# Kernel optimization log

Measured on AMD Instinct MI355X. Metric: run time of the kernel, lower is better.

Reference implementation:

```python
import jax, jax.numpy as jnp
import numpy as np

GAMMA = 2          # relu(cos_sim)**gamma, from init gamma=2
EPS = 1e-8         # torch CosineSimilarity eps (norm clamp)
B, C, H, WID = 4, 256, 64, 64


def setup_inputs() -> dict:
    key = jax.random.key(0)
    kx, kw = jax.random.split(key)
    x = jax.random.normal(kx, (B, C, H, WID), dtype=jnp.float32)
    # 1x1 conv (nlayers=1): weight [C_out, C_in], bias [C_out]
    W = jax.random.normal(kw, (C, C), dtype=jnp.float32) * 0.02
    b = jnp.zeros((C,), dtype=jnp.float32)
    return {"x": x, "W": W, "b": b}


def reference(x, W, b):
    # x: [B,C,H,W]. Flatten pixels: p/q index (h*W+w).
    Bs, Cs, Hs, Ws = x.shape
    xf = x.reshape(Bs, Cs, Hs * Ws)                      # [B,C,P]
    norm = jnp.sqrt(jnp.sum(xf * xf, axis=1, keepdims=True))
    xn = xf / jnp.maximum(norm, EPS)                     # channel-normalized
    # full pairwise cosine similarity over pixels, relu, power gamma
    s = jax.nn.relu(jnp.einsum('bcp,bcq->bpq', xn, xn)) ** GAMMA  # [B,P,Q]
    # transform: 1x1 conv = per-pixel linear map over channels
    gx = jnp.einsum('oc,bcp->bop', W, xf) + b[None, :, None]      # [B,C,P]
    # y[b,c,p] = sum_q s[b,p,q] * gx[b,c,q]  (== 'bijhw,bchw->bcij')
    y = jnp.einsum('bpq,bcq->bcp', s, gx)
    return y.reshape(Bs, Cs, Hs, Ws)
```

## Files before the change

### kernel.cpp

```cpp
#include <hip/hip_runtime.h>

#define BN 4
#define CN 256
#define PN 4096
#define QT 64
#define TSTR 264

typedef __attribute__((ext_vector_type(8))) short short8;
typedef __attribute__((ext_vector_type(8))) unsigned short ushort8;
typedef __attribute__((ext_vector_type(4))) float f32x4;
typedef __attribute__((ext_vector_type(4))) unsigned int u32x4;
typedef unsigned int u32;

__device__ __forceinline__ unsigned short f2bf(float f) {
  u32 u = __builtin_bit_cast(u32, f);
  return (unsigned short)((u + 0x7fffu + ((u >> 16) & 1u)) >> 16);
}

__device__ __forceinline__ void async_copy16(const void* g, void* l) {
  __builtin_amdgcn_global_load_lds((const __attribute__((address_space(1))) u32*)g,
                                   (__attribute__((address_space(3))) u32*)l, 16, 0, 0);
}


__global__ __launch_bounds__(256) void k_nx(const float* __restrict__ x,
                                            float* __restrict__ mnorm,
                                            unsigned short* __restrict__ xnK) {
  __shared__ unsigned short tl[64 * TSTR];
  __shared__ float red[4][64];
  const int b = blockIdx.y, qb = blockIdx.x, p0 = qb * 64;
  const int tid = threadIdx.x;
  const int tp = tid & 63, cg = tid >> 6;
  const float* xp = x + ((size_t)b * CN + cg * 64) * PN + p0 + tp;
  float v[64];
  float ss = 0.f;
#pragma unroll
  for (int i = 0; i < 64; ++i) {
    v[i] = xp[(size_t)i * PN];
    ss += v[i] * v[i];
  }
  red[cg][tp] = ss;
  __syncthreads();
  float nrm = sqrtf(red[0][tp] + red[1][tp] + red[2][tp] + red[3][tp]);
  float mn = fmaxf(nrm, 1e-8f);
  float rn = 1.f / mn;
  if (cg == 0) mnorm[b * PN + p0 + tp] = mn;
  unsigned int* tl32 = (unsigned int*)tl;
#pragma unroll
  for (int j = 0; j < 32; ++j) {
    unsigned int w = (unsigned int)f2bf(v[2 * j] * rn) |
                     ((unsigned int)f2bf(v[2 * j + 1] * rn) << 16);
    tl32[tp * (TSTR / 2) + cg * 32 + j] = w;
  }
  __syncthreads();
  char* dstb = (char*)xnK + (size_t)b * (PN * CN * 2) + (size_t)qb * 32768;
#pragma unroll
  for (int m = 0; m < 8; ++m) {
    int idx = m * 256 + tid;
    int F = idx >> 6, ln = idx & 63;
    int pl = (F >> 3) * 16 + (ln & 15);
    int ch = (F & 7) * 32 + (ln >> 4) * 8;
    ushort8 o = *(const ushort8*)(tl + pl * TSTR + ch);
    *(ushort8*)(dstb + (size_t)idx * 16) = o;
  }
}

__global__ void k_gx(const float* __restrict__ Wm, const float* __restrict__ bias,
                     const unsigned short* __restrict__ xnK, const float* __restrict__ mnorm,
                     unsigned short* __restrict__ gxF) {
  const int b = blockIdx.z;
  const int m0 = blockIdx.y * 64;
  const int qb = blockIdx.x, q0 = qb * 64;
  const int tid = threadIdx.x;
  const int wave = tid >> 6, lane = tid & 63;
  const int lr = lane & 15, g = lane >> 4;

  short8 af[8];
  {
    const float* wr = Wm + (size_t)(m0 + wave * 16 + lr) * CN;
#pragma unroll
    for (int k = 0; k < 8; ++k) {
      const float* ap = wr + k * 32 + g * 8;
      short8 a;
#pragma unroll
      for (int j = 0; j < 8; ++j) a[j] = (short)f2bf(ap[j]);
      af[k] = a;
    }
  }
  f32x4 acc[4];
#pragma unroll
  for (int n = 0; n < 4; ++n) acc[n] = (f32x4){0.f, 0.f, 0.f, 0.f};

  const char* xb = (const char*)xnK + (size_t)b * (PN * CN * 2) + (size_t)qb * 32768;
#pragma unroll
  for (int n = 0; n < 4; ++n)
#pragma unroll
    for (int k = 0; k < 8; ++k) {
      short8 bf = *(const short8*)(xb + ((n * 8 + k) << 10) + ((g * 16 + lr) << 4));
      acc[n] = __builtin_amdgcn_mfma_f32_16x16x32_bf16(af[k], bf, acc[n], 0, 0, 0);
    }
  char* vbb = (char*)gxF + (size_t)b * (PN * CN * 2) + (size_t)qb * 32768;
#pragma unroll
  for (int n = 0; n < 4; ++n) {
    int q = q0 + n * 16 + lr;
    float mn = mnorm[b * PN + q];
    int kk = n >> 1;
    int q32 = (n & 1) * 16 + lr;
    int gp = (q32 >> 2) & 3;
    int j = ((q32 >> 4) & 1) * 4 + (q32 & 3);
#pragma unroll
    for (int i = 0; i < 4; ++i) {
      int c = m0 + wave * 16 + g * 4 + i;
      float v = acc[n][i] * mn + bias[c];
      *(unsigned short*)(vbb + ((kk * 16 + (c >> 4)) << 10) + (gp << 8) + ((c & 15) << 4) + (j << 1)) = f2bf(v);
    }
  }
}

extern __shared__ char smem[];

__global__ __launch_bounds__(512, 2) void k_attn(const unsigned short* __restrict__ xnK,
                                                 const unsigned short* __restrict__ gxF,
                                                 float* __restrict__ d0, float* __restrict__ d1,
                                                 float* __restrict__ d2, float* __restrict__ d3,
                                                 int lq, int ntiles) {
  const int fid = blockIdx.x;
  const int b = fid & 3;
  const int qs = (fid >> 2) & ((1 << lq) - 1);
  const int pblk = fid >> (2 + lq);
  const int tid = threadIdx.x;
  const int wave = tid >> 6, lane = tid & 63, lr = lane & 15, g = lane >> 4;
  const int qb0 = (qs * (PN >> lq)) >> 6;
  const int p0 = pblk * 256 + wave * 32;
  float* dst = (qs == 0) ? d0 : (qs == 1) ? d1 : (qs == 2) ? d2 : d3;

  const char* xb = (const char*)xnK + (size_t)b * (PN * CN * 2);
  const char* vg = (const char*)gxF + (size_t)b * (PN * CN * 2);
  const char* kq = xb + (size_t)qb0 * 32768;
  const char* vq = vg + (size_t)qb0 * 32768;
  const int ldst = tid * 16;
  const int lane16 = lane * 16;

  auto issue_K = [&](int t) {
    char* kb = smem + (t & 1) * 65536;
    const char* s = kq + (size_t)t * 32768 + ldst;
#pragma unroll
    for (int j = 0; j < 4; ++j) async_copy16(s + j * 8192, kb + ldst + j * 8192);
  };
  auto issue_V = [&](int t) {
    char* vb = smem + (t & 1) * 65536 + 32768;
    const char* s = vq + (size_t)t * 32768 + ldst;
#pragma unroll
    for (int j = 0; j < 4; ++j) async_copy16(s + j * 8192, vb + ldst + j * 8192);
  };

  issue_K(0);
  issue_V(0);

  short8 qf[2][8];
  {
    const char* qpb = xb + (size_t)(pblk * 4 + (wave >> 1)) * 32768;
#pragma unroll
    for (int mt = 0; mt < 2; ++mt) {
      int ntp = (wave & 1) * 2 + mt;
#pragma unroll
      for (int k = 0; k < 8; ++k)
        qf[mt][k] = *(const short8*)(qpb + ((ntp * 8 + k) << 10) + ((g * 16 + lr) << 4));
    }
  }

  f32x4 yacc[2][16];
#pragma unroll
  for (int mt = 0; mt < 2; ++mt)
#pragma unroll
    for (int n = 0; n < 16; ++n) yacc[mt][n] = (f32x4){0.f, 0.f, 0.f, 0.f};

  for (int t = 0; t < ntiles; ++t) {
    const char* kb = smem + (t & 1) * 65536;
    const char* vb = kb + 32768;

    asm volatile("s_waitcnt vmcnt(4)" ::: "memory");
    __builtin_amdgcn_s_barrier();
    if (t + 1 < ntiles) { issue_K(t + 1); issue_V(t + 1); }

    u32 pa[2][2][4];
#pragma unroll
    for (int nh = 0; nh < 2; ++nh) {
      f32x4 sacc[2][2];
#pragma unroll
      for (int n0 = 0; n0 < 2; ++n0)
#pragma unroll
        for (int mt = 0; mt < 2; ++mt) sacc[n0][mt] = (f32x4){0.f, 0.f, 0.f, 0.f};
      __builtin_amdgcn_s_setprio(1);
#pragma unroll
      for (int k = 0; k < 8; ++k) {
        short8 kf0 = *(const short8*)(kb + ((2 * nh) * 8 + k) * 1024 + lane16);
        short8 kf1 = *(const short8*)(kb + ((2 * nh + 1) * 8 + k) * 1024 + lane16);
        sacc[0][0] = __builtin_amdgcn_mfma_f32_16x16x32_bf16(kf0, qf[0][k], sacc[0][0], 0, 0, 0);
        sacc[0][1] = __builtin_amdgcn_mfma_f32_16x16x32_bf16(kf0, qf[1][k], sacc[0][1], 0, 0, 0);
        sacc[1][0] = __builtin_amdgcn_mfma_f32_16x16x32_bf16(kf1, qf[0][k], sacc[1][0], 0, 0, 0);
        sacc[1][1] = __builtin_amdgcn_mfma_f32_16x16x32_bf16(kf1, qf[1][k], sacc[1][1], 0, 0, 0);
      }
      __builtin_amdgcn_s_setprio(0);
#pragma unroll
      for (int mt = 0; mt < 2; ++mt)
#pragma unroll
        for (int n0 = 0; n0 < 2; ++n0)
#pragma unroll
          for (int h = 0; h < 2; ++h) {
            float a0 = fmaxf(sacc[n0][mt][2 * h], 0.f);
            a0 *= a0;
            float a1 = fmaxf(sacc[n0][mt][2 * h + 1], 0.f);
            a1 *= a1;
            u32 w;
            asm("v_cvt_pk_bf16_f32 %0, %1, %2" : "=v"(w) : "v"(a0), "v"(a1));
            pa[mt][nh][n0 * 2 + h] = w;
          }
    }

    if (t + 1 < ntiles) {
      asm volatile("s_waitcnt vmcnt(8)" ::: "memory");
    } else {
      asm volatile("s_waitcnt vmcnt(0)" ::: "memory");
    }
    __builtin_amdgcn_s_barrier();

#pragma unroll
    for (int kk = 0; kk < 2; ++kk) {
      u32x4 w0 = {pa[0][kk][0], pa[0][kk][1], pa[0][kk][2], pa[0][kk][3]};
      u32x4 w1 = {pa[1][kk][0], pa[1][kk][1], pa[1][kk][2], pa[1][kk][3]};
      short8 a0 = __builtin_bit_cast(short8, w0);
      short8 a1 = __builtin_bit_cast(short8, w1);
      __builtin_amdgcn_s_setprio(1);
#pragma unroll
      for (int n2 = 0; n2 < 16; ++n2) {
        short8 vf = *(const short8*)(vb + (kk * 16 + n2) * 1024 + lane16);
        yacc[0][n2] = __builtin_amdgcn_mfma_f32_16x16x32_bf16(a0, vf, yacc[0][n2], 0, 0, 0);
        yacc[1][n2] = __builtin_amdgcn_mfma_f32_16x16x32_bf16(a1, vf, yacc[1][n2], 0, 0, 0);
      }
      __builtin_amdgcn_s_setprio(0);
    }
  }
  __builtin_amdgcn_s_barrier();

  float* yl = (float*)(smem + wave * 16384);
  const int row8 = lane >> 3, p4 = (lane & 7) << 2;
#pragma unroll
  for (int cc = 0; cc < 4; ++cc) {
#pragma unroll
    for (int nn = 0; nn < 4; ++nn)
#pragma unroll
      for (int mt = 0; mt < 2; ++mt)
#pragma unroll
        for (int i = 0; i < 4; ++i)
          yl[(nn * 16 + lr) * 33 + mt * 16 + g * 4 + i] = yacc[mt][cc * 4 + nn][i];
#pragma unroll
    for (int r2 = 0; r2 < 8; ++r2) {
      int c = r2 * 8 + row8;
      float4 v = *(const float4*)(yl + c * 33 + p4);
      *(float4*)(dst + ((size_t)b * CN + cc * 64 + c) * PN + p0 + p4) = v;
    }
  }
}

__global__ void k_add(float* __restrict__ o, const float* __restrict__ a,
                      const float* __restrict__ bb, const float* __restrict__ c,
                      int np, int n4) {
  int i = blockIdx.x * blockDim.x + threadIdx.x;
  int stride = gridDim.x * blockDim.x;
  float4* o4 = (float4*)o;
  const float4* a4 = (const float4*)a;
  const float4* b4 = (const float4*)bb;
  const float4* c4 = (const float4*)c;
  for (; i < n4; i += stride) {
    float4 r = o4[i];
    float4 va = a4[i];
    r.x += va.x; r.y += va.y; r.z += va.z; r.w += va.w;
    if (np > 1) {
      float4 vb = b4[i];
      r.x += vb.x; r.y += vb.y; r.z += vb.z; r.w += vb.w;
      float4 vc = c4[i];
      r.x += vc.x; r.y += vc.y; r.z += vc.z; r.w += vc.w;
    }
    o4[i] = r;
  }
}

extern "C" void kernel_launch(void* const* d_in, const int* in_sizes, int n_in,
                              void* d_out, int out_size, void* d_ws, size_t ws_size,
                              hipStream_t stream) {
  const float* x = (const float*)d_in[0];
  const float* Wm = (const float*)d_in[1];
  const float* bias = (const float*)d_in[2];
  float* out = (float*)d_out;

  char* ws = (char*)d_ws;
  unsigned short* xnK = (unsigned short*)ws;
  unsigned short* gxF = (unsigned short*)(ws + (size_t)8388608);
  float* mnorm = (float*)(ws + (size_t)16777216);
  float* yp0 = (float*)(ws + (size_t)16842752);
  float* yp1 = yp0 + 4194304;
  float* yp2 = yp1 + 4194304;
  const size_t need4 = 16842752ULL + 3ULL * 16777216ULL;

  hipFuncSetAttribute(reinterpret_cast<const void*>(k_attn),
                      hipFuncAttributeMaxDynamicSharedMemorySize, 131072);

  k_nx<<<dim3(PN / 64, BN), 256, 0, stream>>>(x, mnorm, xnK);
  k_gx<<<dim3(PN / 64, CN / 64, BN), 256, 0, stream>>>(Wm, bias, xnK, mnorm, gxF);
  if (ws_size >= need4) {
    k_attn<<<dim3(256), 512, 131072, stream>>>(xnK, gxF, out, yp0, yp1, yp2, 2, (PN / 4) / QT);
    k_add<<<dim3(1024), 256, 0, stream>>>(out, yp0, yp1, yp2, 3, BN * CN * PN / 4);
  } else {
    k_attn<<<dim3(128), 512, 131072, stream>>>(xnK, gxF, out, yp0, yp0, yp0, 1, (PN / 2) / QT);
    k_add<<<dim3(1024), 256, 0, stream>>>(out, yp0, yp0, yp0, 1, BN * CN * PN / 4);
  }
}
```

Before: 101.1 us.

## Fuse normalize and 1x1 conv kernels; store split-Q partials in fp16

Merges the normalization kernel and the conv-transform kernel into one. Each block computes the gx tile from its bf16 normalized tile already in LDS, with norms kept in shared memory, instead of re-reading xnK and mnorm from global. The split-Q attention partials are now written as fp16 into four workspace buffers rather than fp32 into the output plus three buffers. The final add kernel converts and sums all four, which roughly halves the partial-sum traffic and removes a launch. The cost is fp16 precision and range on the partial outputs, and each block in the fused kernel now does the whole 256-channel GEMM, with fewer blocks than the old k_gx grid.

```diff
diff --git a/kernel.cpp b/kernel.cpp
--- a/kernel.cpp
+++ b/kernel.cpp
@@ -1,4 +1,5 @@
 #include <hip/hip_runtime.h>
+#include <hip/hip_fp16.h>
 
 #define BN 4
 #define CN 256
@@ -8,6 +9,7 @@
 
 typedef __attribute__((ext_vector_type(8))) short short8;
 typedef __attribute__((ext_vector_type(8))) unsigned short ushort8;
+typedef __attribute__((ext_vector_type(4))) unsigned short us4;
 typedef __attribute__((ext_vector_type(4))) float f32x4;
 typedef __attribute__((ext_vector_type(4))) unsigned int u32x4;
 typedef unsigned int u32;
@@ -23,96 +25,99 @@
 }
 
 
-__global__ __launch_bounds__(256) void k_nx(const float* __restrict__ x,
-                                            float* __restrict__ mnorm,
-                                            unsigned short* __restrict__ xnK) {
+__global__ __launch_bounds__(256) void k_nxgx(const float* __restrict__ x,
+                                              const float* __restrict__ Wm,
+                                              const float* __restrict__ bias,
+                                              unsigned short* __restrict__ xnK,
+                                              unsigned short* __restrict__ gxF) {
   __shared__ unsigned short tl[64 * TSTR];
   __shared__ float red[4][64];
+  __shared__ float mnl[64];
   const int b = blockIdx.y, qb = blockIdx.x, p0 = qb * 64;
   const int tid = threadIdx.x;
   const int tp = tid & 63, cg = tid >> 6;
-  const float* xp = x + ((size_t)b * CN + cg * 64) * PN + p0 + tp;
-  float v[64];
-  float ss = 0.f;
-#pragma unroll
-  for (int i = 0; i < 64; ++i) {
-    v[i] = xp[(size_t)i * PN];
-    ss += v[i] * v[i];
-  }
-  red[cg][tp] = ss;
-  __syncthreads();
-  float nrm = sqrtf(red[0][tp] + red[1][tp] + red[2][tp] + red[3][tp]);
-  float mn = fmaxf(nrm, 1e-8f);
-  float rn = 1.f / mn;
-  if (cg == 0) mnorm[b * PN + p0 + tp] = mn;
-  unsigned int* tl32 = (unsigned int*)tl;
-#pragma unroll
-  for (int j = 0; j < 32; ++j) {
-    unsigned int w = (unsigned int)f2bf(v[2 * j] * rn) |
-                     ((unsigned int)f2bf(v[2 * j + 1] * rn) << 16);
-    tl32[tp * (TSTR / 2) + cg * 32 + j] = w;
-  }
-  __syncthreads();
-  char* dstb = (char*)xnK + (size_t)b * (PN * CN * 2) + (size_t)qb * 32768;
-#pragma unroll
-  for (int m = 0; m < 8; ++m) {
-    int idx = m * 256 + tid;
-    int F = idx >> 6, ln = idx & 63;
-    int pl = (F >> 3) * 16 + (ln & 15);
-    int ch = (F & 7) * 32 + (ln >> 4) * 8;
-    ushort8 o = *(const ushort8*)(tl + pl * TSTR + ch);
-    *(ushort8*)(dstb + (size_t)idx * 16) = o;
-  }
-}
-
-__global__ void k_gx(const float* __restrict__ Wm, const float* __restrict__ bias,
-                     const unsigned short* __restrict__ xnK, const float* __restrict__ mnorm,
-                     unsigned short* __restrict__ gxF) {
-  const int b = blockIdx.z;
-  const int m0 = blockIdx.y * 64;
-  const int qb = blockIdx.x, q0 = qb * 64;
-  const int tid = threadIdx.x;
+
+  {
+    const float* xp = x + ((size_t)b * CN + cg * 64) * PN + p0 + tp;
+    float v[64];
+    float ss = 0.f;
+#pragma unroll
+    for (int i = 0; i < 64; ++i) {
+      v[i] = xp[(size_t)i * PN];
+      ss += v[i] * v[i];
+    }
+    red[cg][tp] = ss;
+    __syncthreads();
+    float nrm = sqrtf(red[0][tp] + red[1][tp] + red[2][tp] + red[3][tp]);
+    float mn = fmaxf(nrm, 1e-8f);
+    float rn = 1.f / mn;
+    if (cg == 0) mnl[tp] = mn;
+    unsigned int* tl32 = (unsigned int*)tl;
+#pragma unroll
+    for (int j = 0; j < 32; ++j) {
+      unsigned int w = (unsigned int)f2bf(v[2 * j] * rn) |
+                       ((unsigned int)f2bf(v[2 * j + 1] * rn) << 16);
+      tl32[tp * (TSTR / 2) + cg * 32 + j] = w;
+    }
+    __syncthreads();
+    char* dstb = (char*)xnK + (size_t)b * (PN * CN * 2) + (size_t)qb * 32768;
+#pragma unroll
+    for (int m = 0; m < 8; ++m) {
+      int idx = m * 256 + tid;
+      int F = idx >> 6, ln = idx & 63;
+      int pl = (F >> 3) * 16 + (ln & 15);
+      int ch = (F & 7) * 32 + (ln >> 4) * 8;
+      ushort8 o = *(const ushort8*)(tl + pl * TSTR + ch);
+      *(ushort8*)(dstb + (size_t)idx * 16) = o;
+    }
+  }
+
   const int wave = tid >> 6, lane = tid & 63;
   const int lr = lane & 15, g = lane >> 4;
-
-  short8 af[8];
-  {
-    const float* wr = Wm + (size_t)(m0 + wave * 16 + lr) * CN;
-#pragma unroll
-    for (int k = 0; k < 8; ++k) {
-      const float* ap = wr + k * 32 + g * 8;
-      short8 a;
-#pragma unroll
-      for (int j = 0; j < 8; ++j) a[j] = (short)f2bf(ap[j]);
-      af[k] = a;
-    }
-  }
-  f32x4 acc[4];
-#pragma unroll
-  for (int n = 0; n < 4; ++n) acc[n] = (f32x4){0.f, 0.f, 0.f, 0.f};
-
-  const char* xb = (const char*)xnK + (size_t)b * (PN * CN * 2) + (size_t)qb * 32768;
-#pragma unroll
-  for (int n = 0; n < 4; ++n)
-#pragma unroll
-    for (int k = 0; k < 8; ++k) {
-      short8 bf = *(const short8*)(xb + ((n * 8 + k) << 10) + ((g * 16 + lr) << 4));
-      acc[n] = __builtin_amdgcn_mfma_f32_16x16x32_bf16(af[k], bf, acc[n], 0, 0, 0);
-    }
   char* vbb = (char*)gxF + (size_t)b * (PN * CN * 2) + (size_t)qb * 32768;
 #pragma unroll
-  for (int n = 0; n < 4; ++n) {
-    int q = q0 + n * 16 + lr;
-    float mn = mnorm[b * PN + q];
-    int kk = n >> 1;
-    int q32 = (n & 1) * 16 + lr;
-    int gp = (q32 >> 2) & 3;
-    int j = ((q32 >> 4) & 1) * 4 + (q32 & 3);
-#pragma unroll
-    for (int i = 0; i < 4; ++i) {
-      int c = m0 + wave * 16 + g * 4 + i;
-      float v = acc[n][i] * mn + bias[c];
-      *(unsigned short*)(vbb + ((kk * 16 + (c >> 4)) << 10) + (gp << 8) + ((c & 15) << 4) + (j << 1)) = f2bf(v);
+  for (int mp = 0; mp < 2; ++mp) {
+    short8 af[2][8];
+#pragma unroll
+    for (int mt = 0; mt < 2; ++mt) {
+      const float* wr = Wm + (size_t)(wave * 64 + mp * 32 + mt * 16 + lr) * CN;
+#pragma unroll
+      for (int k = 0; k < 8; ++k) {
+        const float* ap = wr + k * 32 + g * 8;
+        short8 a;
+#pragma unroll
+        for (int j = 0; j < 8; ++j) a[j] = (short)f2bf(ap[j]);
+        af[mt][k] = a;
+      }
+    }
+    f32x4 acc[2][4];
+#pragma unroll
+    for (int mt = 0; mt < 2; ++mt)
+#pragma unroll
+      for (int n = 0; n < 4; ++n) acc[mt][n] = (f32x4){0.f, 0.f, 0.f, 0.f};
+#pragma unroll
+    for (int n = 0; n < 4; ++n)
+#pragma unroll
+      for (int k = 0; k < 8; ++k) {
+        short8 bf = *(const short8*)((const char*)tl + (n * 16 + lr) * (TSTR * 2) + k * 64 + g * 16);
+        acc[0][n] = __builtin_amdgcn_mfma_f32_16x16x32_bf16(af[0][k], bf, acc[0][n], 0, 0, 0);
+        acc[1][n] = __builtin_amdgcn_mfma_f32_16x16x32_bf16(af[1][k], bf, acc[1][n], 0, 0, 0);
+      }
+#pragma unroll
+    for (int n = 0; n < 4; ++n) {
+      float mn = mnl[n * 16 + lr];
+      int kk = n >> 1;
+      int q32 = (n & 1) * 16 + lr;
+      int gp = (q32 >> 2) & 3;
+      int j = ((q32 >> 4) & 1) * 4 + (q32 & 3);
+#pragma unroll
+      for (int mt = 0; mt < 2; ++mt)
+#pragma unroll
+        for (int i = 0; i < 4; ++i) {
+          int c = wave * 64 + mp * 32 + mt * 16 + g * 4 + i;
+          float v = acc[mt][n][i] * mn + bias[c];
+          *(unsigned short*)(vbb + ((kk * 16 + (c >> 4)) << 10) + (gp << 8) + ((c & 15) << 4) + (j << 1)) = f2bf(v);
+        }
     }
   }
 }
@@ -121,8 +126,8 @@
 
 __global__ __launch_bounds__(512, 2) void k_attn(const unsigned short* __restrict__ xnK,
                                                  const unsigned short* __restrict__ gxF,
-                                                 float* __restrict__ d0, float* __restrict__ d1,
-                                                 float* __restrict__ d2, float* __restrict__ d3,
+                                                 __half* __restrict__ p0h, __half* __restrict__ p1h,
+                                                 __half* __restrict__ p2h, __half* __restrict__ p3h,
                                                  int lq, int ntiles) {
   const int fid = blockIdx.x;
   const int b = fid & 3;
@@ -132,7 +137,7 @@
   const int wave = tid >> 6, lane = tid & 63, lr = lane & 15, g = lane >> 4;
   const int qb0 = (qs * (PN >> lq)) >> 6;
   const int p0 = pblk * 256 + wave * 32;
-  float* dst = (qs == 0) ? d0 : (qs == 1) ? d1 : (qs == 2) ? d2 : d3;
+  __half* dsth = (qs == 0) ? p0h : (qs == 1) ? p1h : (qs == 2) ? p2h : p3h;
 
   const char* xb = (const char*)xnK + (size_t)b * (PN * CN * 2);
   const char* vg = (const char*)gxF + (size_t)b * (PN * CN * 2);
@@ -208,10 +213,8 @@
         for (int n0 = 0; n0 < 2; ++n0)
 #pragma unroll
           for (int h = 0; h < 2; ++h) {
-            float a0 = fmaxf(sacc[n0][mt][2 * h], 0.f);
-            a0 *= a0;
-            float a1 = fmaxf(sacc[n0][mt][2 * h + 1], 0.f);
-            a1 *= a1;
+            float a0 = fmaxf(sacc[n0][mt][2 * h], 0.f); a0 *= a0;
+            float a1 = fmaxf(sacc[n0][mt][2 * h + 1], 0.f); a1 *= a1;
             u32 w;
             asm("v_cvt_pk_bf16_f32 %0, %1, %2" : "=v"(w) : "v"(a0), "v"(a1));
             pa[mt][nh][n0 * 2 + h] = w;
@@ -258,29 +261,41 @@
     for (int r2 = 0; r2 < 8; ++r2) {
       int c = r2 * 8 + row8;
       float4 v = *(const float4*)(yl + c * 33 + p4);
-      *(float4*)(dst + ((size_t)b * CN + cc * 64 + c) * PN + p0 + p4) = v;
-    }
-  }
-}
-
-__global__ void k_add(float* __restrict__ o, const float* __restrict__ a,
-                      const float* __restrict__ bb, const float* __restrict__ c,
-                      int np, int n4) {
+      size_t off = ((size_t)b * CN + cc * 64 + c) * PN + p0 + p4;
+      us4 h;
+      h[0] = __builtin_bit_cast(unsigned short, __float2half(v.x));
+      h[1] = __builtin_bit_cast(unsigned short, __float2half(v.y));
+      h[2] = __builtin_bit_cast(unsigned short, __float2half(v.z));
+      h[3] = __builtin_bit_cast(unsigned short, __float2half(v.w));
+      *(us4*)(dsth + off) = h;
+    }
+  }
+}
+
+__global__ void k_add(float* __restrict__ o, const uint2* __restrict__ a,
+                      const uint2* __restrict__ bb, const uint2* __restrict__ c,
+                      const uint2* __restrict__ d, int np, int n4) {
   int i = blockIdx.x * blockDim.x + threadIdx.x;
   int stride = gridDim.x * blockDim.x;
   float4* o4 = (float4*)o;
-  const float4* a4 = (const float4*)a;
-  const float4* b4 = (const float4*)bb;
-  const float4* c4 = (const float4*)c;
   for (; i < n4; i += stride) {
-    float4 r = o4[i];
-    float4 va = a4[i];
-    r.x += va.x; r.y += va.y; r.z += va.z; r.w += va.w;
-    if (np > 1) {
-      float4 vb = b4[i];
-      r.x += vb.x; r.y += vb.y; r.z += vb.z; r.w += vb.w;
-      float4 vc = c4[i];
-      r.x += vc.x; r.y += vc.y; r.z += vc.z; r.w += vc.w;
+    uint2 ua = a[i];
+    float2 f0 = __half22float2(__builtin_bit_cast(__half2, ua.x));
+    float2 f1 = __half22float2(__builtin_bit_cast(__half2, ua.y));
+    float4 r = {f0.x, f0.y, f1.x, f1.y};
+    uint2 ub = bb[i];
+    f0 = __half22float2(__builtin_bit_cast(__half2, ub.x));
+    f1 = __half22float2(__builtin_bit_cast(__half2, ub.y));
+    r.x += f0.x; r.y += f0.y; r.z += f1.x; r.w += f1.y;
+    if (np > 2) {
+      uint2 uc = c[i];
+      f0 = __half22float2(__builtin_bit_cast(__half2, uc.x));
+      f1 = __half22float2(__builtin_bit_cast(__half2, uc.y));
+      r.x += f0.x; r.y += f0.y; r.z += f1.x; r.w += f1.y;
+      uint2 ud = d[i];
+      f0 = __half22float2(__builtin_bit_cast(__half2, ud.x));
+      f1 = __half22float2(__builtin_bit_cast(__half2, ud.y));
+      r.x += f0.x; r.y += f0.y; r.z += f1.x; r.w += f1.y;
     }
     o4[i] = r;
   }
@@ -297,22 +312,23 @@
   char* ws = (char*)d_ws;
   unsigned short* xnK = (unsigned short*)ws;
   unsigned short* gxF = (unsigned short*)(ws + (size_t)8388608);
-  float* mnorm = (float*)(ws + (size_t)16777216);
-  float* yp0 = (float*)(ws + (size_t)16842752);
-  float* yp1 = yp0 + 4194304;
-  float* yp2 = yp1 + 4194304;
-  const size_t need4 = 16842752ULL + 3ULL * 16777216ULL;
+  __half* p0 = (__half*)(ws + (size_t)16777216);
+  __half* p1 = p0 + 4194304;
+  __half* p2 = p1 + 4194304;
+  __half* p3 = p2 + 4194304;
+  const size_t need4 = 16777216ULL + 4ULL * 8388608ULL;
 
   hipFuncSetAttribute(reinterpret_cast<const void*>(k_attn),
                       hipFuncAttributeMaxDynamicSharedMemorySize, 131072);
 
-  k_nx<<<dim3(PN / 64, BN), 256, 0, stream>>>(x, mnorm, xnK);
-  k_gx<<<dim3(PN / 64, CN / 64, BN), 256, 0, stream>>>(Wm, bias, xnK, mnorm, gxF);
+  k_nxgx<<<dim3(PN / 64, BN), 256, 0, stream>>>(x, Wm, bias, xnK, gxF);
   if (ws_size >= need4) {
-    k_attn<<<dim3(256), 512, 131072, stream>>>(xnK, gxF, out, yp0, yp1, yp2, 2, (PN / 4) / QT);
-    k_add<<<dim3(1024), 256, 0, stream>>>(out, yp0, yp1, yp2, 3, BN * CN * PN / 4);
+    k_attn<<<dim3(256), 512, 131072, stream>>>(xnK, gxF, p0, p1, p2, p3, 2, (PN / 4) / QT);
+    k_add<<<dim3(1024), 256, 0, stream>>>(out, (const uint2*)p0, (const uint2*)p1,
+                                          (const uint2*)p2, (const uint2*)p3, 4, BN * CN * PN / 4);
   } else {
-    k_attn<<<dim3(128), 512, 131072, stream>>>(xnK, gxF, out, yp0, yp0, yp0, 1, (PN / 2) / QT);
-    k_add<<<dim3(1024), 256, 0, stream>>>(out, yp0, yp0, yp0, 1, BN * CN * PN / 4);
-  }
-}
+    k_attn<<<dim3(128), 512, 131072, stream>>>(xnK, gxF, p0, p1, p0, p1, 1, (PN / 2) / QT);
+    k_add<<<dim3(1024), 256, 0, stream>>>(out, (const uint2*)p0, (const uint2*)p1,
+                                          (const uint2*)p0, (const uint2*)p1, 2, BN * CN * PN / 4);
+  }
+}
```

Result: faster. 94.67 us (-6.4%).
